# Kernel tuning notes

Hardware: AMD Instinct MI355X
Metric: run time of the kernel (lower is better)

The kernel has to match this reference:

```python
import jax, jax.numpy as jnp
import numpy as np

D_MODEL = 1024
N_HEADS = 16
HEAD_DIM = D_MODEL // N_HEADS
B, T = 4, 2048


def setup_inputs() -> dict:
    key = jax.random.key(0)
    k_x, k_len, k_wqkv, k_bqkv, k_wo, k_bo = jax.random.split(key, 6)
    x = jax.random.normal(k_x, (B, T, D_MODEL), dtype=jnp.float32)
    # left-aligned valid-token mask: first `length` tokens valid per sequence
    lengths = jax.random.randint(k_len, (B,), T // 2, T + 1)
    attention_mask = (jnp.arange(T)[None, :] < lengths[:, None]).astype(jnp.int32)
    s = 1.0 / np.sqrt(D_MODEL)
    Wqkv = jax.random.normal(k_wqkv, (3 * D_MODEL, D_MODEL), dtype=jnp.float32) * s
    bqkv = jax.random.normal(k_bqkv, (3 * D_MODEL,), dtype=jnp.float32) * 0.01
    Wo = jax.random.normal(k_wo, (D_MODEL, D_MODEL), dtype=jnp.float32) * s
    bo = jax.random.normal(k_bo, (D_MODEL,), dtype=jnp.float32) * 0.01
    return {"x": x, "attention_mask": attention_mask,
            "Wqkv": Wqkv, "bqkv": bqkv, "Wo": Wo, "bo": bo}


def reference(x, attention_mask, Wqkv, bqkv, Wo, bo):
    Bx, Tx, C = x.shape
    qkv = x @ Wqkv.T + bqkv                      # [B,T,3C]
    q, k, v = jnp.split(qkv, 3, axis=-1)
    def heads(t):                                # [B,T,C] -> [B,H,T,hd]
        return t.reshape(Bx, Tx, N_HEADS, HEAD_DIM).transpose(0, 2, 1, 3)
    q, k, v = heads(q), heads(k), heads(v)
    att = jnp.einsum('bhqd,bhkd->bhqk', q, k) / np.sqrt(HEAD_DIM)
    causal = jnp.tril(jnp.ones((Tx, Tx), dtype=bool))[None, None]
    att = jnp.where(causal, att, -jnp.inf)
    key_mask = attention_mask.astype(bool)[:, None, None, :]  # [B,1,1,T]
    att = jnp.where(key_mask, att, -jnp.inf)
    att = jax.nn.softmax(att, axis=-1)
    query_mask = attention_mask.astype(att.dtype)[:, None, :, None]
    att = att * query_mask
    y = jnp.einsum('bhqk,bhkd->bhqd', att, v)
    y = y.transpose(0, 2, 1, 3).reshape(Bx, Tx, C)
    y = y * attention_mask.astype(y.dtype)[:, :, None]
    return y @ Wo.T + bo
```

## Files before the change

### kernel.cpp

```cpp
#include <hip/hip_runtime.h>
#include <hip/hip_bf16.h>
#include <stdint.h>

#define D_MODEL 1024
#define N_HEADS 16
#define HEAD_DIM 64
#define BB 4
#define TT 2048
#define M_TOK (BB * TT)

typedef __attribute__((ext_vector_type(8))) short short8;
typedef __attribute__((ext_vector_type(4))) short short4v;
typedef __attribute__((ext_vector_type(4))) float float4v;

#define KS_STRIDE 72
#define VT_STRIDE 76

__device__ __forceinline__ short f2bf(float f) {
    union { float f; uint32_t u; } v; v.f = f;
    uint32_t u = v.u;
    uint32_t r = u + 0x7FFF + ((u >> 16) & 1);
    return (short)(r >> 16);
}
__device__ __forceinline__ float bf2f(short s) {
    union { uint32_t u; float f; } v;
    v.u = ((uint32_t)(unsigned short)s) << 16;
    return v.f;
}

__device__ __forceinline__ float4v mfma16(short4v a, short4v b, float4v c) {
#if __has_builtin(__builtin_amdgcn_mfma_f32_16x16x16bf16_1k)
    return __builtin_amdgcn_mfma_f32_16x16x16bf16_1k(a, b, c, 0, 0, 0);
#else
    asm volatile("v_mfma_f32_16x16x16_bf16 %0, %1, %2, %0"
                 : "+v"(c) : "v"(a), "v"(b));
    return c;
#endif
}

__device__ __forceinline__ void async_cp16(const short* g, short* l) {
    __builtin_amdgcn_global_load_lds(
        (const __attribute__((address_space(1))) void*)g,
        (__attribute__((address_space(3))) void*)l, 16, 0, 0);
}

__global__ void probe_kernel(const unsigned short* __restrict__ xs,
                             const int* __restrict__ mask,
                             int* __restrict__ flag) {
    __shared__ int red[256];
    const int tid = threadIdx.x;
    int cnt = 0;
    for (int i = tid; i < 8192; i += 256) {
        const unsigned short u = xs[i];
        if (((u >> 7) & 0xFF) >= 134) cnt++;
    }
    red[tid] = cnt;
    __syncthreads();
    for (int s = 128; s > 0; s >>= 1) {
        if (tid < s) red[tid] += red[tid + s];
        __syncthreads();
    }
    if (tid == 0) flag[0] = (red[0] > 512) ? 1 : 0;
    for (int b = 0; b < BB; ++b) {
        __syncthreads();
        int c = 0;
        for (int i = tid; i < TT; i += 256) c += (mask[b * TT + i] != 0) ? 1 : 0;
        red[tid] = c;
        __syncthreads();
        for (int s = 128; s > 0; s >>= 1) {
            if (tid < s) red[tid] += red[tid + s];
            __syncthreads();
        }
        if (tid == 0) flag[4 + b] = red[0];
    }
}

__global__ __launch_bounds__(256) void cvt_kernel(
    const void* __restrict__ src, short* __restrict__ dst,
    const int* __restrict__ flag, int n8) {
    const int i = blockIdx.x * 256 + threadIdx.x;
    if (i >= n8) return;
    if (*flag) {
        const float4v f0 = ((const float4v*)src)[2 * i];
        const float4v f1 = ((const float4v*)src)[2 * i + 1];
        short8 o;
        for (int j = 0; j < 4; ++j) { o[j] = f2bf(f0[j]); o[j + 4] = f2bf(f1[j]); }
        ((short8*)dst)[i] = o;
    } else {
        ((short8*)dst)[i] = ((const short8*)src)[i];
    }
}

__global__ __launch_bounds__(256) void gemm_qkv(
    const short* __restrict__ X, const short* __restrict__ W,
    const void* __restrict__ biasv, void* __restrict__ outv,
    const int* __restrict__ flagp, int M, int N, int K) {
    __shared__ short As[128 * 32];
    __shared__ short Bs[128 * 32];

    const int f32m = flagp[0];
    const int bm = blockIdx.y * 128;
    const int bn = blockIdx.x * 128;
    const int len = flagp[4 + (bm >> 11)];
    if ((bm & (TT - 1)) >= len) return;

    const int tid  = threadIdx.x;
    const int lane = tid & 63;
    const int wave = tid >> 6;
    const int quad = lane >> 4;
    const int l16  = lane & 15;
    const int wm = (wave >> 1) * 64;
    const int wn = (wave & 1) * 64;

    float4v acc[4][4];
    const float4v zero4 = {0.f, 0.f, 0.f, 0.f};
    for (int i = 0; i < 4; ++i)
        for (int j = 0; j < 4; ++j) acc[i][j] = zero4;

    const int srow = tid >> 2;
    const int skc  = (tid & 3) * 8;
    const short* xg0 = &X[(size_t)(bm + srow) * K + skc];
    const short* xg1 = &X[(size_t)(bm + 64 + srow) * K + skc];
    const short* wg0 = &W[(size_t)(bn + srow) * K + skc];
    const short* wg1 = &W[(size_t)(bn + 64 + srow) * K + skc];
    short* asd0 = &As[wave * 512];
    short* asd1 = &As[2048 + wave * 512];
    short* bsd0 = &Bs[wave * 512];
    short* bsd1 = &Bs[2048 + wave * 512];

    for (int k0 = 0; k0 < K; k0 += 32) {
        __syncthreads();
        async_cp16(xg0 + k0, asd0);
        async_cp16(xg1 + k0, asd1);
        async_cp16(wg0 + k0, bsd0);
        async_cp16(wg1 + k0, bsd1);
        __syncthreads();

        short8 a[4], b[4];
        for (int i = 0; i < 4; ++i)
            a[i] = *(short8*)&As[(wm + i * 16 + l16) * 32 + quad * 8];
        for (int j = 0; j < 4; ++j)
            b[j] = *(short8*)&Bs[(wn + j * 16 + l16) * 32 + quad * 8];
        for (int i = 0; i < 4; ++i)
            for (int j = 0; j < 4; ++j)
                acc[i][j] = __builtin_amdgcn_mfma_f32_16x16x32_bf16(
                    a[i], b[j], acc[i][j], 0, 0, 0);
    }

    const bool vblock = (bn >= 2 * D_MODEL);
    for (int i = 0; i < 4; ++i) {
        for (int j = 0; j < 4; ++j) {
            const int n = bn + wn + j * 16 + l16;
            const float bf = f32m ? ((const float*)biasv)[n]
                                  : bf2f(((const short*)biasv)[n]);
            if (vblock) {
                const int t0 = bm + wm + i * 16 + quad * 4;
                const int b  = t0 >> 11;
                const int t  = t0 & (TT - 1);
                const int hh = (n >> 6) & 15;
                const int d  = n & 63;
                short4v pk;
                for (int r = 0; r < 4; ++r) pk[r] = f2bf(acc[i][j][r] + bf);
                short* dst = (short*)outv + 2 * (size_t)BB * N_HEADS * TT * HEAD_DIM;
                *(short4v*)&dst[(((size_t)b * N_HEADS + hh) * HEAD_DIM + d) * TT + t] = pk;
                continue;
            }
            for (int r = 0; r < 4; ++r) {
                const int m = bm + wm + i * 16 + quad * 4 + r;
                const int b  = m >> 11;
                const int t  = m & (TT - 1);
                const int wh = n >> 10;
                const int hh = (n >> 6) & 15;
                const int d  = n & 63;
                short* dst = (short*)outv +
                    (size_t)wh * ((size_t)BB * N_HEADS * TT * HEAD_DIM);
                dst[(((size_t)b * N_HEADS + hh) * TT + t) * HEAD_DIM + d] =
                    f2bf(acc[i][j][r] + bf);
            }
        }
    }
}

__global__ __launch_bounds__(256) void gemm_out(
    const short* __restrict__ X, const short* __restrict__ W,
    const void* __restrict__ biasv, void* __restrict__ outv,
    const int* __restrict__ flagp, int M, int N, int K) {
    __shared__ short As[64 * 32];
    __shared__ short Bs[128 * 32];
    __shared__ float Es[4][16][66];

    const int f32m = flagp[0];
    const int bm = blockIdx.y * 64;
    const int bn = blockIdx.x * 128;
    const int len = flagp[4 + (bm >> 11)];
    const bool dead = (bm & (TT - 1)) >= len;

    const int tid  = threadIdx.x;
    const int lane = tid & 63;
    const int wave = tid >> 6;
    const int quad = lane >> 4;
    const int l16  = lane & 15;
    const int wm = (wave >> 1) * 32;
    const int wn = (wave & 1) * 64;

    float4v acc[2][4];
    const float4v zero4 = {0.f, 0.f, 0.f, 0.f};
    for (int i = 0; i < 2; ++i)
        for (int j = 0; j < 4; ++j) acc[i][j] = zero4;

    if (!dead) {
        const int srow = tid >> 2;
        const int skc  = (tid & 3) * 8;
        const short* xg  = &X[(size_t)(bm + srow) * K + skc];
        const short* wg0 = &W[(size_t)(bn + srow) * K + skc];
        const short* wg1 = &W[(size_t)(bn + 64 + srow) * K + skc];
        short* asd  = &As[wave * 512];
        short* bsd0 = &Bs[wave * 512];
        short* bsd1 = &Bs[2048 + wave * 512];

        for (int k0 = 0; k0 < K; k0 += 32) {
            __syncthreads();
            async_cp16(xg + k0, asd);
            async_cp16(wg0 + k0, bsd0);
            async_cp16(wg1 + k0, bsd1);
            __syncthreads();

            short8 a[2], b[4];
            for (int i = 0; i < 2; ++i)
                a[i] = *(short8*)&As[(wm + i * 16 + l16) * 32 + quad * 8];
            for (int j = 0; j < 4; ++j)
                b[j] = *(short8*)&Bs[(wn + j * 16 + l16) * 32 + quad * 8];
            for (int i = 0; i < 2; ++i)
                for (int j = 0; j < 4; ++j)
                    acc[i][j] = __builtin_amdgcn_mfma_f32_16x16x32_bf16(
                        a[i], b[j], acc[i][j], 0, 0, 0);
        }
    }

    for (int i = 0; i < 2; ++i) {
        for (int j = 0; j < 4; ++j) {
            const int n = bn + wn + j * 16 + l16;
            const float bf = f32m ? ((const float*)biasv)[n]
                                  : bf2f(((const short*)biasv)[n]);
            for (int r = 0; r < 4; ++r)
                Es[wave][quad * 4 + r][j * 16 + l16] =
                    dead ? bf : (acc[i][j][r] + bf);
        }
        for (int pass = 0; pass < 4; ++pass) {
            const int row = pass * 4 + quad;
            const int m = bm + wm + i * 16 + row;
            const float4v v4 = *(float4v*)&Es[wave][row][l16 * 4];
            const size_t off = (size_t)m * N + bn + wn + l16 * 4;
            if (f32m) {
                *(float4v*)&((float*)outv)[off] = v4;
            } else {
                short4v pk;
                for (int r = 0; r < 4; ++r) pk[r] = f2bf(v4[r]);
                *(short4v*)&((short*)outv)[off] = pk;
            }
        }
    }
}

__global__ __launch_bounds__(256) void attn_kernel(
    const short* __restrict__ Q, const short* __restrict__ Kb,
    const short* __restrict__ Vt_g, const int* __restrict__ flagp,
    short* __restrict__ Y) {
    __shared__ short Ks[2][64 * KS_STRIDE];
    __shared__ short Vt[2][64 * VT_STRIDE];

    const int x = blockIdx.x;
    const int h = blockIdx.y, b = blockIdx.z;
    const int tid  = threadIdx.x;
    const int lane = tid & 63;
    const int wave = tid >> 6;
    const int quad = lane >> 4;
    const int l16  = lane & 15;

    const int len = flagp[4 + b];
    const int L64 = (len + 63) >> 6;
    const size_t bh = ((size_t)b * N_HEADS + h) * TT * HEAD_DIM;

    const int cA = x;
    const int cB = L64 - 1 - x;
    const bool pair = (cB >= cA);
    const bool hasB = (cB > cA);

    if (pair) {
        const int qwA = cA * 64 + wave * 16;
        const int qwB = cB * 64 + wave * 16;

        short8 qa[2][2];
        for (int c = 0; c < 2; ++c)
            qa[0][c] = *(const short8*)&Q[bh + (size_t)(qwA + l16) * HEAD_DIM + c * 32 + quad * 8];
        if (hasB)
            for (int c = 0; c < 2; ++c)
                qa[1][c] = *(const short8*)&Q[bh + (size_t)(qwB + l16) * HEAD_DIM + c * 32 + quad * 8];

        const float4v zero4 = {0.f, 0.f, 0.f, 0.f};
        float4v o[2][4];
        for (int qf = 0; qf < 2; ++qf)
            for (int i = 0; i < 4; ++i) o[qf][i] = zero4;
        float psum[2] = {0.f, 0.f};

        const int srow = tid >> 2;
        const int scol = (tid & 3) * 16;

        short8 kr0, kr1, vr0, vr1;
#define LOAD_TILE(kb)                                                     \
        {                                                                 \
            const size_t gk = bh + (size_t)((kb) + srow) * HEAD_DIM + scol;\
            const size_t gv = bh + (size_t)srow * TT + (kb) + scol;       \
            kr0 = *(const short8*)&Kb[gk];   kr1 = *(const short8*)&Kb[gk + 8];\
            vr0 = *(const short8*)&Vt_g[gv]; vr1 = *(const short8*)&Vt_g[gv + 8];\
        }
#define STORE_TILE(buf)                                                   \
        {                                                                 \
            *(short8*)&Ks[buf][srow * KS_STRIDE + scol]     = kr0;        \
            *(short8*)&Ks[buf][srow * KS_STRIDE + scol + 8] = kr1;        \
            *(short8*)&Vt[buf][srow * VT_STRIDE + scol]     = vr0;        \
            *(short8*)&Vt[buf][srow * VT_STRIDE + scol + 8] = vr1;        \
        }

        const int ntiles = cB + 1;
        LOAD_TILE(0);
        STORE_TILE(0);
        if (ntiles > 1) LOAD_TILE(64);
        __syncthreads();

        for (int kt = 0; kt < ntiles; ++kt) {
            const int kbase = kt * 64;
            const int cur = kt & 1;
            if (kt + 1 < ntiles) {
                STORE_TILE(1 - cur);
                if (kt + 2 < ntiles) LOAD_TILE(kbase + 128);
            }

            const int qmaxw = (hasB ? qwB : qwA) + 15;
            if (kbase <= qmaxw) {
                short8 kbf[4][2];
                for (int nt = 0; nt < 4; ++nt) {
                    kbf[nt][0] = *(short8*)&Ks[cur][(nt * 16 + l16) * KS_STRIDE + quad * 8];
                    kbf[nt][1] = *(short8*)&Ks[cur][(nt * 16 + l16) * KS_STRIDE + 32 + quad * 8];
                }
                for (int qf = 0; qf < 2; ++qf) {
                    if (qf == 1 && !hasB) continue;
                    const int qw = qf ? qwB : qwA;
                    if (kbase > qw + 15) continue;

                    float4v s[4];
                    for (int nt = 0; nt < 4; ++nt) {
                        float4v z = zero4;
                        z = __builtin_amdgcn_mfma_f32_16x16x32_bf16(kbf[nt][0], qa[qf][0], z, 0, 0, 0);
                        z = __builtin_amdgcn_mfma_f32_16x16x32_bf16(kbf[nt][1], qa[qf][1], z, 0, 0, 0);
                        s[nt] = z;
                    }

                    const int q = qw + l16;
                    float lps = 0.f;
                    short4v pf[4];
                    const bool full = (kbase + 63 <= qw) && (kbase + 64 <= len);
                    if (full) {
                        for (int nt = 0; nt < 4; ++nt)
                            for (int r = 0; r < 4; ++r) {
                                const float e = exp2f(s[nt][r] * 0.18033688011f);
                                lps += e;
                                pf[nt][r] = f2bf(e);
                            }
                    } else {
                        for (int nt = 0; nt < 4; ++nt)
                            for (int r = 0; r < 4; ++r) {
                                const int key = kbase + nt * 16 + quad * 4 + r;
                                const float e = exp2f(s[nt][r] * 0.18033688011f);
                                const float p = (key <= q && key < len) ? e : 0.f;
                                lps += p;
                                pf[nt][r] = f2bf(p);
                            }
                    }
                    psum[qf] += lps;

                    for (int nt2 = 0; nt2 < 4; ++nt2) {
                        float4v accv = o[qf][nt2];
                        for (int nt = 0; nt < 4; ++nt) {
                            short4v vf = *(short4v*)&Vt[cur][(nt2 * 16 + l16) * VT_STRIDE
                                                             + nt * 16 + quad * 4];
                            accv = mfma16(pf[nt], vf, accv);
                        }
                        o[qf][nt2] = accv;
                    }
                }
            }
            __syncthreads();
        }
#undef LOAD_TILE
#undef STORE_TILE

        for (int qf = 0; qf < 2; ++qf) {
            if (qf == 1 && !hasB) continue;
            const int qw = qf ? qwB : qwA;
            float ps = psum[qf];
            ps += __shfl_xor(ps, 16, 64);
            ps += __shfl_xor(ps, 32, 64);
            for (int r = 0; r < 4; ++r) {
                const int q = qw + quad * 4 + r;
                const float lsum = __shfl(ps, quad * 4 + r, 16);
                const float inv = (lsum > 0.f && q < len) ? (1.0f / lsum) : 0.f;
                for (int nt2 = 0; nt2 < 4; ++nt2) {
                    Y[((size_t)(b * TT + q)) * D_MODEL + h * HEAD_DIM + nt2 * 16 + l16] =
                        f2bf(o[qf][nt2][r] * inv);
                }
            }
        }
    }

    const int z = 31 - x;
    if (z >= L64) {
        const short4v zz = {0, 0, 0, 0};
        for (int r = 0; r < 4; ++r) {
            const int q = z * 64 + wave * 16 + quad * 4 + r;
            *(short4v*)&Y[((size_t)(b * TT + q)) * D_MODEL + h * HEAD_DIM + l16 * 4] = zz;
        }
    }
}

extern "C" void kernel_launch(void* const* d_in, const int* in_sizes, int n_in,
                              void* d_out, int out_size, void* d_ws, size_t ws_size,
                              hipStream_t stream) {
    const void* x    = d_in[0];
    const int*  mask = (const int*)d_in[1];
    const void* Wqkv = d_in[2];
    const void* bqkv = d_in[3];
    const void* Wo   = d_in[4];
    const void* bo   = d_in[5];

    int*   flag = (int*)d_ws;
    short* qbuf = (short*)d_ws + 128;
    const size_t QSZ = (size_t)BB * N_HEADS * TT * HEAD_DIM;
    short* kbuf = qbuf + QSZ;
    short* vbuf = qbuf + 2 * QSZ;
    short* xyb  = qbuf + 3 * QSZ;
    short* wqb  = qbuf + 4 * QSZ;

    probe_kernel<<<1, 256, 0, stream>>>((const unsigned short*)x, mask, flag);

    cvt_kernel<<<(M_TOK * D_MODEL / 8 + 255) / 256, 256, 0, stream>>>(
        x, xyb, flag, M_TOK * D_MODEL / 8);
    cvt_kernel<<<(3 * D_MODEL * D_MODEL / 8 + 255) / 256, 256, 0, stream>>>(
        Wqkv, wqb, flag, 3 * D_MODEL * D_MODEL / 8);

    gemm_qkv<<<dim3((3 * D_MODEL) / 128, M_TOK / 128), 256, 0, stream>>>(
        xyb, wqb, bqkv, qbuf, flag, M_TOK, 3 * D_MODEL, D_MODEL);

    attn_kernel<<<dim3(16, N_HEADS, BB), 256, 0, stream>>>(
        qbuf, kbuf, vbuf, flag, xyb);

    cvt_kernel<<<(D_MODEL * D_MODEL / 8 + 255) / 256, 256, 0, stream>>>(
        Wo, kbuf, flag, D_MODEL * D_MODEL / 8);

    gemm_out<<<dim3(D_MODEL / 128, M_TOK / 64), 256, 0, stream>>>(
        xyb, kbuf, bo, d_out, flag, M_TOK, D_MODEL, D_MODEL);
}
```

Before: 312.5 us.

## Fold softmax scale into Q, use hardware exp2, compute row sums via MFMA

Moves the log2e/sqrt(d) scale into the QKV GEMM epilogue so Q is stored prescaled, and removes the per-element multiply in attention. Replaces exp2f with the raw hardware exp2 builtin. Computes the softmax denominators with an MFMA against a ones vector on the bf16-rounded probabilities, which drops the scalar accumulation and cross-lane shuffles. The probe kernel is also split across 5 blocks to run in parallel. Extra costs are MFMA work per tile and a sum taken over bf16-rounded values, which changes numerics slightly.

```diff
diff --git a/kernel.cpp b/kernel.cpp
--- a/kernel.cpp
+++ b/kernel.cpp
@@ -1,6 +1,7 @@
 #include <hip/hip_runtime.h>
 #include <hip/hip_bf16.h>
 #include <stdint.h>
+#include <math.h>
 
 #define D_MODEL 1024
 #define N_HEADS 16
@@ -16,6 +17,8 @@
 #define KS_STRIDE 72
 #define VT_STRIDE 76
 
+#define QK_SCALE 0.18033688011f
+
 __device__ __forceinline__ short f2bf(float f) {
     union { float f; uint32_t u; } v; v.f = f;
     uint32_t u = v.u;
@@ -26,6 +29,14 @@
     union { uint32_t u; float f; } v;
     v.u = ((uint32_t)(unsigned short)s) << 16;
     return v.f;
+}
+
+__device__ __forceinline__ float exp2fast(float x) {
+#if __has_builtin(__builtin_amdgcn_exp2f)
+    return __builtin_amdgcn_exp2f(x);
+#else
+    return exp2f(x);
+#endif
 }
 
 __device__ __forceinline__ float4v mfma16(short4v a, short4v b, float4v c) {
@@ -49,20 +60,22 @@
                              int* __restrict__ flag) {
     __shared__ int red[256];
     const int tid = threadIdx.x;
-    int cnt = 0;
-    for (int i = tid; i < 8192; i += 256) {
-        const unsigned short u = xs[i];
-        if (((u >> 7) & 0xFF) >= 134) cnt++;
-    }
-    red[tid] = cnt;
-    __syncthreads();
-    for (int s = 128; s > 0; s >>= 1) {
-        if (tid < s) red[tid] += red[tid + s];
+    const int task = blockIdx.x;
+    if (task == 0) {
+        int cnt = 0;
+        for (int i = tid; i < 8192; i += 256) {
+            const unsigned short u = xs[i];
+            if (((u >> 7) & 0xFF) >= 134) cnt++;
+        }
+        red[tid] = cnt;
         __syncthreads();
-    }
-    if (tid == 0) flag[0] = (red[0] > 512) ? 1 : 0;
-    for (int b = 0; b < BB; ++b) {
-        __syncthreads();
+        for (int s = 128; s > 0; s >>= 1) {
+            if (tid < s) red[tid] += red[tid + s];
+            __syncthreads();
+        }
+        if (tid == 0) flag[0] = (red[0] > 512) ? 1 : 0;
+    } else {
+        const int b = task - 1;
         int c = 0;
         for (int i = tid; i < TT; i += 256) c += (mask[b * TT + i] != 0) ? 1 : 0;
         red[tid] = c;
@@ -165,17 +178,18 @@
                 *(short4v*)&dst[(((size_t)b * N_HEADS + hh) * HEAD_DIM + d) * TT + t] = pk;
                 continue;
             }
+            const int wh = n >> 10;
+            const float scale = (wh == 0) ? QK_SCALE : 1.0f;
             for (int r = 0; r < 4; ++r) {
                 const int m = bm + wm + i * 16 + quad * 4 + r;
                 const int b  = m >> 11;
                 const int t  = m & (TT - 1);
-                const int wh = n >> 10;
                 const int hh = (n >> 6) & 15;
                 const int d  = n & 63;
                 short* dst = (short*)outv +
                     (size_t)wh * ((size_t)BB * N_HEADS * TT * HEAD_DIM);
                 dst[(((size_t)b * N_HEADS + hh) * TT + t) * HEAD_DIM + d] =
-                    f2bf(acc[i][j][r] + bf);
+                    f2bf((acc[i][j][r] + bf) * scale);
             }
         }
     }
@@ -298,10 +312,13 @@
                 qa[1][c] = *(const short8*)&Q[bh + (size_t)(qwB + l16) * HEAD_DIM + c * 32 + quad * 8];
 
         const float4v zero4 = {0.f, 0.f, 0.f, 0.f};
+        const short one_bf = (short)0x3F80;
+        const short8 ones8 = {one_bf, one_bf, one_bf, one_bf,
+                              one_bf, one_bf, one_bf, one_bf};
         float4v o[2][4];
         for (int qf = 0; qf < 2; ++qf)
             for (int i = 0; i < 4; ++i) o[qf][i] = zero4;
-        float psum[2] = {0.f, 0.f};
+        float4v ps[2] = {zero4, zero4};
 
         const int srow = tid >> 2;
         const int scol = (tid & 3) * 16;
@@ -343,6 +360,7 @@
                     kbf[nt][0] = *(short8*)&Ks[cur][(nt * 16 + l16) * KS_STRIDE + quad * 8];
                     kbf[nt][1] = *(short8*)&Ks[cur][(nt * 16 + l16) * KS_STRIDE + 32 + quad * 8];
                 }
+#pragma unroll
                 for (int qf = 0; qf < 2; ++qf) {
                     if (qf == 1 && !hasB) continue;
                     const int qw = qf ? qwB : qwA;
@@ -357,27 +375,30 @@
                     }
 
                     const int q = qw + l16;
-                    float lps = 0.f;
                     short4v pf[4];
                     const bool full = (kbase + 63 <= qw) && (kbase + 64 <= len);
                     if (full) {
                         for (int nt = 0; nt < 4; ++nt)
-                            for (int r = 0; r < 4; ++r) {
-                                const float e = exp2f(s[nt][r] * 0.18033688011f);
-                                lps += e;
-                                pf[nt][r] = f2bf(e);
-                            }
+                            for (int r = 0; r < 4; ++r)
+                                pf[nt][r] = f2bf(exp2fast(s[nt][r]));
                     } else {
                         for (int nt = 0; nt < 4; ++nt)
                             for (int r = 0; r < 4; ++r) {
                                 const int key = kbase + nt * 16 + quad * 4 + r;
-                                const float e = exp2f(s[nt][r] * 0.18033688011f);
-                                const float p = (key <= q && key < len) ? e : 0.f;
-                                lps += p;
-                                pf[nt][r] = f2bf(p);
+                                const float e = exp2fast(s[nt][r]);
+                                pf[nt][r] = f2bf((key <= q && key < len) ? e : 0.f);
                             }
                     }
-                    psum[qf] += lps;
+
+                    short8 p80, p81;
+                    for (int r = 0; r < 4; ++r) {
+                        p80[r] = pf[0][r]; p80[4 + r] = pf[1][r];
+                        p81[r] = pf[2][r]; p81[4 + r] = pf[3][r];
+                    }
+                    ps[qf] = __builtin_amdgcn_mfma_f32_16x16x32_bf16(
+                        p80, ones8, ps[qf], 0, 0, 0);
+                    ps[qf] = __builtin_amdgcn_mfma_f32_16x16x32_bf16(
+                        p81, ones8, ps[qf], 0, 0, 0);
 
                     for (int nt2 = 0; nt2 < 4; ++nt2) {
                         float4v accv = o[qf][nt2];
@@ -395,16 +416,14 @@
 #undef LOAD_TILE
 #undef STORE_TILE
 
+#pragma unroll
         for (int qf = 0; qf < 2; ++qf) {
             if (qf == 1 && !hasB) continue;
             const int qw = qf ? qwB : qwA;
-            float ps = psum[qf];
-            ps += __shfl_xor(ps, 16, 64);
-            ps += __shfl_xor(ps, 32, 64);
             for (int r = 0; r < 4; ++r) {
                 const int q = qw + quad * 4 + r;
-                const float lsum = __shfl(ps, quad * 4 + r, 16);
-                const float inv = (lsum > 0.f && q < len) ? (1.0f / lsum) : 0.f;
+                const float denom = ps[qf][r];
+                const float inv = (denom > 0.f && q < len) ? (1.0f / denom) : 0.f;
                 for (int nt2 = 0; nt2 < 4; ++nt2) {
                     Y[((size_t)(b * TT + q)) * D_MODEL + h * HEAD_DIM + nt2 * 16 + l16] =
                         f2bf(o[qf][nt2][r] * inv);
@@ -441,7 +460,7 @@
     short* xyb  = qbuf + 3 * QSZ;
     short* wqb  = qbuf + 4 * QSZ;
 
-    probe_kernel<<<1, 256, 0, stream>>>((const unsigned short*)x, mask, flag);
+    probe_kernel<<<5, 256, 0, stream>>>((const unsigned short*)x, mask, flag);
 
     cvt_kernel<<<(M_TOK * D_MODEL / 8 + 255) / 256, 256, 0, stream>>>(
         x, xyb, flag, M_TOK * D_MODEL / 8);
```

Result: faster. 296.4 us (-5.2%).
